# Kernel tuning notes

Measured on AMD Instinct MI355X. Metric: run time of the kernel, lower is better.

The kernel has to match this reference:

```python
import jax, jax.numpy as jnp
import numpy as np

D_MODEL = 512
N_PAIRS = D_MODEL // 2
B, T = 8, 4096


def setup_inputs() -> dict:
    key = jax.random.key(0)
    ks = jax.random.split(key, 7)
    scale = 1.0 / np.sqrt(D_MODEL)
    return {
        "x_seq": jax.random.normal(ks[0], (B, T, D_MODEL), dtype=jnp.float32),
        "W_angle": jax.random.uniform(ks[1], (D_MODEL, N_PAIRS), jnp.float32, -scale, scale),
        "b_angle": jnp.zeros((N_PAIRS,), jnp.float32),
        "W_decay": jax.random.uniform(ks[2], (D_MODEL, 1), jnp.float32, -scale, scale),
        "b_decay": jnp.full((1,), 1.4, jnp.float32),
        "W_input": jax.random.uniform(ks[3], (D_MODEL, D_MODEL), jnp.float32, -scale, scale),
        "b_input": jax.random.uniform(ks[4], (D_MODEL,), jnp.float32, -scale, scale),
    }


def _givens_ssm(x_seq, W_angle, b_angle, W_decay, b_decay, W_input, b_input):
    Bb, Tt, D = x_seq.shape
    P = D // 2
    angles = jnp.einsum("btd,dp->btp", x_seq, W_angle) + b_angle          # [B,T,P]
    decays = jax.nn.sigmoid(jnp.einsum("btd,dk->btk", x_seq, W_decay) + b_decay)[..., 0]  # [B,T]
    inj = jnp.einsum("btd,de->bte", x_seq, W_input) + b_input              # [B,T,D]
    inj = inj.reshape(Bb, Tt, P, 2)

    # scan over time: h_t = decay_t * Rot(angles_t) h_{t-1} + inj_t, pairwise 2x2 rotations
    def step(h, inp):
        a, d, u = inp  # a:[B,P], d:[B], u:[B,P,2]
        c, s = jnp.cos(a), jnp.sin(a)
        he = c * h[..., 0] - s * h[..., 1]
        ho = s * h[..., 0] + c * h[..., 1]
        h_new = d[:, None, None] * jnp.stack([he, ho], axis=-1) + u
        return h_new, h_new

    h0 = jnp.zeros((Bb, P, 2), x_seq.dtype)
    xs = (jnp.swapaxes(angles, 0, 1), jnp.swapaxes(decays, 0, 1), jnp.swapaxes(inj, 0, 1))
    _, states = jax.lax.scan(step, h0, xs)  # [T,B,P,2]
    return jnp.swapaxes(states, 0, 1).reshape(Bb, Tt, D)


def reference(x_seq, W_angle, b_angle, W_decay, b_decay, W_input, b_input):
    return _givens_ssm(x_seq, W_angle, b_angle, W_decay, b_decay, W_input, b_input)
```

## Files before the change

kernel.cpp:

```cpp
#include <hip/hip_runtime.h>
#include <math.h>

typedef _Float16 half_t;
typedef __attribute__((ext_vector_type(8))) _Float16 half8;
typedef __attribute__((ext_vector_type(4))) _Float16 half4;
typedef __attribute__((ext_vector_type(2))) _Float16 half2v;
typedef __attribute__((ext_vector_type(4))) float floatx4;

#define BATCH   8
#define SEQ     4096
#define DM      512
#define NP      256
#define M_TOT   32768
#define NTOT    768
#define CHUNKS  128
#define CHUNK_LEN 32

__device__ __forceinline__ void async_load16(const void* g, void* l) {
    __builtin_amdgcn_global_load_lds((const __attribute__((address_space(1))) void*)g,
                                     (__attribute__((address_space(3))) void*)l,
                                     16, 0, 0);
}

__global__ __launch_bounds__(256) void decay_convert(const float* __restrict__ X,
                                                     const float* __restrict__ Wd,
                                                     const float* __restrict__ bd,
                                                     float* __restrict__ dec,
                                                     half_t* __restrict__ Xh) {
    const int wave = threadIdx.x >> 6;
    const int lane = threadIdx.x & 63;
    const int row  = blockIdx.x * 4 + wave;
    const float4* xr = (const float4*)(X + (size_t)row * DM);
    const float4* wd = (const float4*)Wd;
    float4 v0 = xr[2 * lane], v1 = xr[2 * lane + 1];
    float4 w0 = wd[2 * lane], w1 = wd[2 * lane + 1];
    float sum = v0.x * w0.x + v0.y * w0.y + v0.z * w0.z + v0.w * w0.w
              + v1.x * w1.x + v1.y * w1.y + v1.z * w1.z + v1.w * w1.w;
    half8 h = {(half_t)v0.x, (half_t)v0.y, (half_t)v0.z, (half_t)v0.w,
               (half_t)v1.x, (half_t)v1.y, (half_t)v1.z, (half_t)v1.w};
    *(half8*)(Xh + (size_t)row * DM + lane * 8) = h;
#pragma unroll
    for (int off = 32; off > 0; off >>= 1) sum += __shfl_down(sum, off, 64);
    if (lane == 0) {
        float z = sum + bd[0];
        dec[row] = 1.0f / (1.0f + __expf(-z));
    }
}

__global__ __launch_bounds__(256) void wcat_transpose(const float* __restrict__ Wi,
                                                      const float* __restrict__ Wa,
                                                      half_t* __restrict__ Wt) {
    const int idx = blockIdx.x * 256 + threadIdx.x;
    const int n = idx >> 9;
    const int k = idx & 511;
    float v = (n < DM) ? Wi[(size_t)k * DM + n] : Wa[(size_t)k * NP + (n - DM)];
    Wt[idx] = (half_t)v;
}

__global__ __launch_bounds__(256) void gemm_fused(const half_t* __restrict__ Xh,
                                                  const half_t* __restrict__ Wt,
                                                  const float* __restrict__ bi,
                                                  const float* __restrict__ ba,
                                                  float* __restrict__ out,
                                                  half_t* __restrict__ angles) {
    __shared__ __align__(16) char As[2][8192];
    __shared__ __align__(16) char Bs[2][8192];

    const int bm   = blockIdx.x;
    const int bn   = blockIdx.y;
    const int tid  = threadIdx.x;
    const int wave = tid >> 6;
    const int lane = tid & 63;
    const int quad = lane >> 4;
    const int l16  = lane & 15;
    const int wrow = wave >> 1;
    const int wcol = wave & 1;

    floatx4 acc[4][4];
#pragma unroll
    for (int i = 0; i < 4; ++i)
#pragma unroll
        for (int j = 0; j < 4; ++j) acc[i][j] = (floatx4){0.f, 0.f, 0.f, 0.f};

    const int s0 = wave * 128 + lane;
    const int s1 = s0 + 64;
    const int r0 = s0 >> 2, kql0 = (s0 & 3) ^ ((r0 >> 1) & 3);
    const int r1 = s1 >> 2, kql1 = (s1 & 3) ^ ((r1 >> 1) & 3);
    const half_t* gA0 = Xh + (size_t)(bm * 128 + r0) * DM + kql0 * 8;
    const half_t* gA1 = Xh + (size_t)(bm * 128 + r1) * DM + kql1 * 8;
    const half_t* gB0 = Wt + (size_t)(bn * 128 + r0) * DM + kql0 * 8;
    const half_t* gB1 = Wt + (size_t)(bn * 128 + r1) * DM + kql1 * 8;

    for (int k0 = 0; k0 < DM; k0 += 64) {
#pragma unroll
        for (int kb = 0; kb < 2; ++kb) {
            const int ko = k0 + kb * 32;
            async_load16(gA0 + ko, As[kb] + wave * 2048);
            async_load16(gA1 + ko, As[kb] + wave * 2048 + 1024);
            async_load16(gB0 + ko, Bs[kb] + wave * 2048);
            async_load16(gB1 + ko, Bs[kb] + wave * 2048 + 1024);
        }
        __syncthreads();

#pragma unroll
        for (int kb = 0; kb < 2; ++kb) {
            half8 af[4], bf[4];
#pragma unroll
            for (int mt = 0; mt < 4; ++mt) {
                const int r = wrow * 64 + mt * 16 + l16;
                af[mt] = *(const half8*)(As[kb] + r * 64 + ((quad ^ ((r >> 1) & 3)) << 4));
            }
#pragma unroll
            for (int nt = 0; nt < 4; ++nt) {
                const int r = wcol * 64 + nt * 16 + l16;
                bf[nt] = *(const half8*)(Bs[kb] + r * 64 + ((quad ^ ((r >> 1) & 3)) << 4));
            }
#pragma unroll
            for (int mt = 0; mt < 4; ++mt)
#pragma unroll
                for (int nt = 0; nt < 4; ++nt)
                    acc[mt][nt] = __builtin_amdgcn_mfma_f32_16x16x32_f16(af[mt], bf[nt],
                                                                         acc[mt][nt], 0, 0, 0);
        }
        __syncthreads();
    }

    const int colbase = bn * 128 + wcol * 64;
#pragma unroll
    for (int nt = 0; nt < 4; ++nt) {
        const int col = colbase + nt * 16 + l16;
        const bool is_inj = col < DM;
        const float bias = is_inj ? bi[col] : ba[col - DM];
#pragma unroll
        for (int mt = 0; mt < 4; ++mt) {
            const int rowb = bm * 128 + wrow * 64 + mt * 16 + quad * 4;
#pragma unroll
            for (int r = 0; r < 4; ++r) {
                const float v = acc[mt][nt][r] + bias;
                const int row = rowb + r;
                if (is_inj) out[(size_t)row * DM + col] = v;
                else        angles[(size_t)row * NP + (col - DM)] = (half_t)v;
            }
        }
    }
}

__global__ __launch_bounds__(256) void scan_sum1(const half_t* __restrict__ angles,
                                                 const float* __restrict__ decays,
                                                 const float* __restrict__ inj,
                                                 float* __restrict__ thetaC,
                                                 float4* __restrict__ hend,
                                                 float* __restrict__ Dprod) {
    const int b    = blockIdx.x >> 6;
    const int sub  = threadIdx.x >> 7;
    const int th   = threadIdx.x & 127;
    const int c    = (blockIdx.x & 63) * 2 + sub;
    const int p0   = th * 2;
    const int t0   = c * CHUNK_LEN;
    const float4* inj4 = (const float4*)inj;

    float h0a = 0, h1a = 0, h0b = 0, h1b = 0, tha = 0, thb = 0, dc = 1.0f;
#pragma unroll 4
    for (int i = 0; i < CHUNK_LEN; ++i) {
        const int t = t0 + i;
        const size_t base = (size_t)(b * SEQ + t) * NP + p0;
        half2v av = *(const half2v*)(angles + base);
        float4 u = inj4[base >> 1];
        float d = decays[b * SEQ + t];
        float a0 = (float)av[0], a1 = (float)av[1];
        float s0, c0, s1, c1;
        __sincosf(a0, &s0, &c0);
        __sincosf(a1, &s1, &c1);
        float n0a = fmaf(d, c0 * h0a - s0 * h1a, u.x);
        float n1a = fmaf(d, s0 * h0a + c0 * h1a, u.y);
        float n0b = fmaf(d, c1 * h0b - s1 * h1b, u.z);
        float n1b = fmaf(d, s1 * h0b + c1 * h1b, u.w);
        h0a = n0a; h1a = n1a; h0b = n0b; h1b = n1b;
        tha += a0; thb += a1; dc *= d;
    }
    const size_t cbase = (size_t)(b * CHUNKS + c) * NP + p0;
    *(float2*)(thetaC + cbase) = make_float2(tha, thb);
    hend[cbase >> 1] = make_float4(h0a, h1a, h0b, h1b);
    if (th == 0) Dprod[b * CHUNKS + c] = dc;
}

__global__ __launch_bounds__(128) void scan_chunks(const float* __restrict__ thetaC,
                                                   const float4* __restrict__ hend,
                                                   const float* __restrict__ Dprod,
                                                   float4* __restrict__ hentry) {
    const int b  = blockIdx.x;
    const int p0 = threadIdx.x * 2;
    float h0a = 0, h1a = 0, h0b = 0, h1b = 0;
    for (int c = 0; c < CHUNKS; ++c) {
        const size_t cbase = (size_t)(b * CHUNKS + c) * NP + p0;
        hentry[cbase >> 1] = make_float4(h0a, h1a, h0b, h1b);
        float2 th2 = *(const float2*)(thetaC + cbase);
        float D = Dprod[b * CHUNKS + c];
        float4 he = hend[cbase >> 1];
        float s0, c0, s1, c1;
        __sincosf(th2.x, &s0, &c0);
        __sincosf(th2.y, &s1, &c1);
        float n0a = fmaf(D, c0 * h0a - s0 * h1a, he.x);
        float n1a = fmaf(D, s0 * h0a + c0 * h1a, he.y);
        float n0b = fmaf(D, c1 * h0b - s1 * h1b, he.z);
        float n1b = fmaf(D, s1 * h0b + c1 * h1b, he.w);
        h0a = n0a; h1a = n1a; h0b = n0b; h1b = n1b;
    }
}

__global__ __launch_bounds__(256) void scan_final(const half_t* __restrict__ angles,
                                                  const float* __restrict__ decays,
                                                  const float4* __restrict__ hentry,
                                                  float* __restrict__ out) {
    const int b    = blockIdx.x >> 6;
    const int sub  = threadIdx.x >> 7;
    const int th   = threadIdx.x & 127;
    const int c    = (blockIdx.x & 63) * 2 + sub;
    const int p0   = th * 2;
    const int t0   = c * CHUNK_LEN;
    float4* out4 = (float4*)out;

    float4 v = hentry[((size_t)(b * CHUNKS + c) * NP + p0) >> 1];
    float h0a = v.x, h1a = v.y, h0b = v.z, h1b = v.w;
#pragma unroll 4
    for (int i = 0; i < CHUNK_LEN; ++i) {
        const int t = t0 + i;
        const size_t base = (size_t)(b * SEQ + t) * NP + p0;
        half2v av = *(const half2v*)(angles + base);
        float4 u = out4[base >> 1];
        float d = decays[b * SEQ + t];
        float a0 = (float)av[0], a1 = (float)av[1];
        float s0, c0, s1, c1;
        __sincosf(a0, &s0, &c0);
        __sincosf(a1, &s1, &c1);
        float n0a = fmaf(d, c0 * h0a - s0 * h1a, u.x);
        float n1a = fmaf(d, s0 * h0a + c0 * h1a, u.y);
        float n0b = fmaf(d, c1 * h0b - s1 * h1b, u.z);
        float n1b = fmaf(d, s1 * h0b + c1 * h1b, u.w);
        h0a = n0a; h1a = n1a; h0b = n0b; h1b = n1b;
        out4[base >> 1] = make_float4(h0a, h1a, h0b, h1b);
    }
}

extern "C" void kernel_launch(void* const* d_in, const int* in_sizes, int n_in,
                              void* d_out, int out_size, void* d_ws, size_t ws_size,
                              hipStream_t stream) {
    const float* x  = (const float*)d_in[0];
    const float* Wa = (const float*)d_in[1];
    const float* ba = (const float*)d_in[2];
    const float* Wd = (const float*)d_in[3];
    const float* bd = (const float*)d_in[4];
    const float* Wi = (const float*)d_in[5];
    const float* bi = (const float*)d_in[6];
    float* out = (float*)d_out;

    char* ws = (char*)d_ws;
    half_t* x_h     = (half_t*)(ws);
    float*  thetaC  = (float*)(ws);
    float4* hend    = (float4*)(ws + 1048576);
    float*  Dprod   = (float*)(ws + 3145728);
    float4* hentry  = (float4*)(ws + 3149824);
    half_t* angles  = (half_t*)(ws + 33554432);
    float*  decays  = (float*)(ws + 50331648);
    half_t* Wcat_t  = (half_t*)(ws + 50462720);

    decay_convert<<<M_TOT / 4, 256, 0, stream>>>(x, Wd, bd, decays, x_h);
    wcat_transpose<<<(NTOT * DM) / 256, 256, 0, stream>>>(Wi, Wa, Wcat_t);
    gemm_fused<<<dim3(M_TOT / 128, NTOT / 128), 256, 0, stream>>>(x_h, Wcat_t, bi, ba, out, angles);

    scan_sum1<<<BATCH * CHUNKS / 2, 256, 0, stream>>>(angles, decays, out, thetaC, hend, Dprod);
    scan_chunks<<<BATCH, 128, 0, stream>>>(thetaC, hend, Dprod, hentry);
    scan_final<<<BATCH * CHUNKS / 2, 256, 0, stream>>>(angles, decays, hentry, out);
}
```

Before: 236.2 us.

## Prefetch scan inputs in register double-buffers, shrink GEMM LDS, two rows per wave

The three scan kernels now load their per-timestep inputs (angles, injections, decays, chunk summaries) in groups of 8 or 4 into register double-buffers, so global-load latency overlaps with the serial recurrence. The GEMM drops from a 64-wide K step with two LDS buffers to a 32-wide K step with one buffer per operand. That halves LDS use, but it also doubles the number of barriers. decay_convert now handles two rows per wave and launches half as many blocks. The prefetching raises register pressure in the scan kernels.

Result: faster. 221.4 us (-6.3%).

```diff
diff --git a/kernel.cpp b/kernel.cpp
--- a/kernel.cpp
+++ b/kernel.cpp
@@ -3,7 +3,6 @@
 
 typedef _Float16 half_t;
 typedef __attribute__((ext_vector_type(8))) _Float16 half8;
-typedef __attribute__((ext_vector_type(4))) _Float16 half4;
 typedef __attribute__((ext_vector_type(2))) _Float16 half2v;
 typedef __attribute__((ext_vector_type(4))) float floatx4;
 
@@ -29,21 +28,31 @@
                                                      half_t* __restrict__ Xh) {
     const int wave = threadIdx.x >> 6;
     const int lane = threadIdx.x & 63;
-    const int row  = blockIdx.x * 4 + wave;
-    const float4* xr = (const float4*)(X + (size_t)row * DM);
+    const int row0 = blockIdx.x * 8 + wave * 2;
+    const float4* x0 = (const float4*)(X + (size_t)row0 * DM);
+    const float4* x1 = x0 + 128;
     const float4* wd = (const float4*)Wd;
-    float4 v0 = xr[2 * lane], v1 = xr[2 * lane + 1];
+    float4 a0 = x0[2 * lane], a1 = x0[2 * lane + 1];
+    float4 b0 = x1[2 * lane], b1 = x1[2 * lane + 1];
     float4 w0 = wd[2 * lane], w1 = wd[2 * lane + 1];
-    float sum = v0.x * w0.x + v0.y * w0.y + v0.z * w0.z + v0.w * w0.w
-              + v1.x * w1.x + v1.y * w1.y + v1.z * w1.z + v1.w * w1.w;
-    half8 h = {(half_t)v0.x, (half_t)v0.y, (half_t)v0.z, (half_t)v0.w,
-               (half_t)v1.x, (half_t)v1.y, (half_t)v1.z, (half_t)v1.w};
-    *(half8*)(Xh + (size_t)row * DM + lane * 8) = h;
-#pragma unroll
-    for (int off = 32; off > 0; off >>= 1) sum += __shfl_down(sum, off, 64);
+    float s0 = a0.x * w0.x + a0.y * w0.y + a0.z * w0.z + a0.w * w0.w
+             + a1.x * w1.x + a1.y * w1.y + a1.z * w1.z + a1.w * w1.w;
+    float s1 = b0.x * w0.x + b0.y * w0.y + b0.z * w0.z + b0.w * w0.w
+             + b1.x * w1.x + b1.y * w1.y + b1.z * w1.z + b1.w * w1.w;
+    half8 h0 = {(half_t)a0.x, (half_t)a0.y, (half_t)a0.z, (half_t)a0.w,
+                (half_t)a1.x, (half_t)a1.y, (half_t)a1.z, (half_t)a1.w};
+    half8 h1 = {(half_t)b0.x, (half_t)b0.y, (half_t)b0.z, (half_t)b0.w,
+                (half_t)b1.x, (half_t)b1.y, (half_t)b1.z, (half_t)b1.w};
+    *(half8*)(Xh + (size_t)row0 * DM + lane * 8) = h0;
+    *(half8*)(Xh + (size_t)(row0 + 1) * DM + lane * 8) = h1;
+#pragma unroll
+    for (int off = 32; off > 0; off >>= 1) {
+        s0 += __shfl_down(s0, off, 64);
+        s1 += __shfl_down(s1, off, 64);
+    }
     if (lane == 0) {
-        float z = sum + bd[0];
-        dec[row] = 1.0f / (1.0f + __expf(-z));
+        dec[row0]     = 1.0f / (1.0f + __expf(-(s0 + bd[0])));
+        dec[row0 + 1] = 1.0f / (1.0f + __expf(-(s1 + bd[0])));
     }
 }
 
@@ -63,8 +72,8 @@
                                                   const float* __restrict__ ba,
                                                   float* __restrict__ out,
                                                   half_t* __restrict__ angles) {
-    __shared__ __align__(16) char As[2][8192];
-    __shared__ __align__(16) char Bs[2][8192];
+    __shared__ __align__(16) char As[8192];
+    __shared__ __align__(16) char Bs[8192];
 
     const int bm   = blockIdx.x;
     const int bn   = blockIdx.y;
@@ -90,38 +99,35 @@
     const half_t* gA1 = Xh + (size_t)(bm * 128 + r1) * DM + kql1 * 8;
     const half_t* gB0 = Wt + (size_t)(bn * 128 + r0) * DM + kql0 * 8;
     const half_t* gB1 = Wt + (size_t)(bn * 128 + r1) * DM + kql1 * 8;
-
-    for (int k0 = 0; k0 < DM; k0 += 64) {
-#pragma unroll
-        for (int kb = 0; kb < 2; ++kb) {
-            const int ko = k0 + kb * 32;
-            async_load16(gA0 + ko, As[kb] + wave * 2048);
-            async_load16(gA1 + ko, As[kb] + wave * 2048 + 1024);
-            async_load16(gB0 + ko, Bs[kb] + wave * 2048);
-            async_load16(gB1 + ko, Bs[kb] + wave * 2048 + 1024);
-        }
+    char* lA0 = As + wave * 2048;
+    char* lA1 = As + wave * 2048 + 1024;
+    char* lB0 = Bs + wave * 2048;
+    char* lB1 = Bs + wave * 2048 + 1024;
+
+    for (int k0 = 0; k0 < DM; k0 += 32) {
+        async_load16(gA0 + k0, lA0);
+        async_load16(gA1 + k0, lA1);
+        async_load16(gB0 + k0, lB0);
+        async_load16(gB1 + k0, lB1);
         __syncthreads();
 
-#pragma unroll
-        for (int kb = 0; kb < 2; ++kb) {
-            half8 af[4], bf[4];
-#pragma unroll
-            for (int mt = 0; mt < 4; ++mt) {
-                const int r = wrow * 64 + mt * 16 + l16;
-                af[mt] = *(const half8*)(As[kb] + r * 64 + ((quad ^ ((r >> 1) & 3)) << 4));
-            }
-#pragma unroll
-            for (int nt = 0; nt < 4; ++nt) {
-                const int r = wcol * 64 + nt * 16 + l16;
-                bf[nt] = *(const half8*)(Bs[kb] + r * 64 + ((quad ^ ((r >> 1) & 3)) << 4));
-            }
-#pragma unroll
-            for (int mt = 0; mt < 4; ++mt)
-#pragma unroll
-                for (int nt = 0; nt < 4; ++nt)
-                    acc[mt][nt] = __builtin_amdgcn_mfma_f32_16x16x32_f16(af[mt], bf[nt],
-                                                                         acc[mt][nt], 0, 0, 0);
-        }
+        half8 af[4], bf[4];
+#pragma unroll
+        for (int mt = 0; mt < 4; ++mt) {
+            const int r = wrow * 64 + mt * 16 + l16;
+            af[mt] = *(const half8*)(As + r * 64 + ((quad ^ ((r >> 1) & 3)) << 4));
+        }
+#pragma unroll
+        for (int nt = 0; nt < 4; ++nt) {
+            const int r = wcol * 64 + nt * 16 + l16;
+            bf[nt] = *(const half8*)(Bs + r * 64 + ((quad ^ ((r >> 1) & 3)) << 4));
+        }
+#pragma unroll
+        for (int mt = 0; mt < 4; ++mt)
+#pragma unroll
+            for (int nt = 0; nt < 4; ++nt)
+                acc[mt][nt] = __builtin_amdgcn_mfma_f32_16x16x32_f16(af[mt], bf[nt],
+                                                                     acc[mt][nt], 0, 0, 0);
         __syncthreads();
     }
 
@@ -151,32 +157,53 @@
                                                  float* __restrict__ thetaC,
                                                  float4* __restrict__ hend,
                                                  float* __restrict__ Dprod) {
-    const int b    = blockIdx.x >> 6;
-    const int sub  = threadIdx.x >> 7;
-    const int th   = threadIdx.x & 127;
-    const int c    = (blockIdx.x & 63) * 2 + sub;
-    const int p0   = th * 2;
-    const int t0   = c * CHUNK_LEN;
-    const float4* inj4 = (const float4*)inj;
+    const int b   = blockIdx.x >> 6;
+    const int sub = threadIdx.x >> 7;
+    const int th  = threadIdx.x & 127;
+    const int c   = (blockIdx.x & 63) * 2 + sub;
+    const int p0  = th * 2;
+    const int t0  = c * CHUNK_LEN;
+
+    const half_t* ap = angles + (size_t)(b * SEQ + t0) * NP + p0;
+    const float4* up = (const float4*)inj + (size_t)(b * SEQ + t0) * 128 + (p0 >> 1);
+    const float*  dp = decays + b * SEQ + t0;
+
+    half2v ab[2][8]; float4 ub[2][8]; float db[2][8];
+#pragma unroll
+    for (int j = 0; j < 8; ++j) {
+        ab[0][j] = *(const half2v*)(ap + (size_t)j * NP);
+        ub[0][j] = up[(size_t)j * 128];
+        db[0][j] = dp[j];
+    }
 
     float h0a = 0, h1a = 0, h0b = 0, h1b = 0, tha = 0, thb = 0, dc = 1.0f;
-#pragma unroll 4
-    for (int i = 0; i < CHUNK_LEN; ++i) {
-        const int t = t0 + i;
-        const size_t base = (size_t)(b * SEQ + t) * NP + p0;
-        half2v av = *(const half2v*)(angles + base);
-        float4 u = inj4[base >> 1];
-        float d = decays[b * SEQ + t];
-        float a0 = (float)av[0], a1 = (float)av[1];
-        float s0, c0, s1, c1;
-        __sincosf(a0, &s0, &c0);
-        __sincosf(a1, &s1, &c1);
-        float n0a = fmaf(d, c0 * h0a - s0 * h1a, u.x);
-        float n1a = fmaf(d, s0 * h0a + c0 * h1a, u.y);
-        float n0b = fmaf(d, c1 * h0b - s1 * h1b, u.z);
-        float n1b = fmaf(d, s1 * h0b + c1 * h1b, u.w);
-        h0a = n0a; h1a = n1a; h0b = n0b; h1b = n1b;
-        tha += a0; thb += a1; dc *= d;
+#pragma unroll
+    for (int g = 0; g < 4; ++g) {
+        const int cur = g & 1, nxt = cur ^ 1;
+        if (g < 3) {
+#pragma unroll
+            for (int j = 0; j < 8; ++j) {
+                const int t = (g + 1) * 8 + j;
+                ab[nxt][j] = *(const half2v*)(ap + (size_t)t * NP);
+                ub[nxt][j] = up[(size_t)t * 128];
+                db[nxt][j] = dp[t];
+            }
+        }
+#pragma unroll
+        for (int j = 0; j < 8; ++j) {
+            float a0 = (float)ab[cur][j][0], a1 = (float)ab[cur][j][1];
+            float4 u = ub[cur][j];
+            float d  = db[cur][j];
+            float s0, c0, s1, c1;
+            __sincosf(a0, &s0, &c0);
+            __sincosf(a1, &s1, &c1);
+            float n0a = fmaf(d, c0 * h0a - s0 * h1a, u.x);
+            float n1a = fmaf(d, s0 * h0a + c0 * h1a, u.y);
+            float n0b = fmaf(d, c1 * h0b - s1 * h1b, u.z);
+            float n1b = fmaf(d, s1 * h0b + c1 * h1b, u.w);
+            h0a = n0a; h1a = n1a; h0b = n0b; h1b = n1b;
+            tha += a0; thb += a1; dc *= d;
+        }
     }
     const size_t cbase = (size_t)(b * CHUNKS + c) * NP + p0;
     *(float2*)(thetaC + cbase) = make_float2(tha, thb);
@@ -190,21 +217,48 @@
                                                    float4* __restrict__ hentry) {
     const int b  = blockIdx.x;
     const int p0 = threadIdx.x * 2;
+    const float2* tp = (const float2*)thetaC + (size_t)b * CHUNKS * 128 + (p0 >> 1);
+    const float4* hp = hend + (size_t)b * CHUNKS * 128 + (p0 >> 1);
+    float4*       ep = hentry + (size_t)b * CHUNKS * 128 + (p0 >> 1);
+    const float*  Dp = Dprod + b * CHUNKS;
+
+    float2 tb[2][4]; float4 hb[2][4]; float Db[2][4];
+#pragma unroll
+    for (int j = 0; j < 4; ++j) {
+        tb[0][j] = tp[(size_t)j * 128];
+        hb[0][j] = hp[(size_t)j * 128];
+        Db[0][j] = Dp[j];
+    }
+
     float h0a = 0, h1a = 0, h0b = 0, h1b = 0;
-    for (int c = 0; c < CHUNKS; ++c) {
-        const size_t cbase = (size_t)(b * CHUNKS + c) * NP + p0;
-        hentry[cbase >> 1] = make_float4(h0a, h1a, h0b, h1b);
-        float2 th2 = *(const float2*)(thetaC + cbase);
-        float D = Dprod[b * CHUNKS + c];
-        float4 he = hend[cbase >> 1];
-        float s0, c0, s1, c1;
-        __sincosf(th2.x, &s0, &c0);
-        __sincosf(th2.y, &s1, &c1);
-        float n0a = fmaf(D, c0 * h0a - s0 * h1a, he.x);
-        float n1a = fmaf(D, s0 * h0a + c0 * h1a, he.y);
-        float n0b = fmaf(D, c1 * h0b - s1 * h1b, he.z);
-        float n1b = fmaf(D, s1 * h0b + c1 * h1b, he.w);
-        h0a = n0a; h1a = n1a; h0b = n0b; h1b = n1b;
+#pragma unroll
+    for (int g = 0; g < 32; ++g) {
+        const int cur = g & 1, nxt = cur ^ 1;
+        if (g < 31) {
+#pragma unroll
+            for (int j = 0; j < 4; ++j) {
+                const int c = (g + 1) * 4 + j;
+                tb[nxt][j] = tp[(size_t)c * 128];
+                hb[nxt][j] = hp[(size_t)c * 128];
+                Db[nxt][j] = Dp[c];
+            }
+        }
+#pragma unroll
+        for (int j = 0; j < 4; ++j) {
+            const int c = g * 4 + j;
+            ep[(size_t)c * 128] = make_float4(h0a, h1a, h0b, h1b);
+            float2 th2 = tb[cur][j];
+            float4 he  = hb[cur][j];
+            float D    = Db[cur][j];
+            float s0, c0, s1, c1;
+            __sincosf(th2.x, &s0, &c0);
+            __sincosf(th2.y, &s1, &c1);
+            float n0a = fmaf(D, c0 * h0a - s0 * h1a, he.x);
+            float n1a = fmaf(D, s0 * h0a + c0 * h1a, he.y);
+            float n0b = fmaf(D, c1 * h0b - s1 * h1b, he.z);
+            float n1b = fmaf(D, s1 * h0b + c1 * h1b, he.w);
+            h0a = n0a; h1a = n1a; h0b = n0b; h1b = n1b;
+        }
     }
 }
 
@@ -212,33 +266,56 @@
                                                   const float* __restrict__ decays,
                                                   const float4* __restrict__ hentry,
                                                   float* __restrict__ out) {
-    const int b    = blockIdx.x >> 6;
-    const int sub  = threadIdx.x >> 7;
-    const int th   = threadIdx.x & 127;
-    const int c    = (blockIdx.x & 63) * 2 + sub;
-    const int p0   = th * 2;
-    const int t0   = c * CHUNK_LEN;
-    float4* out4 = (float4*)out;
-
-    float4 v = hentry[((size_t)(b * CHUNKS + c) * NP + p0) >> 1];
+    const int b   = blockIdx.x >> 6;
+    const int sub = threadIdx.x >> 7;
+    const int th  = threadIdx.x & 127;
+    const int c   = (blockIdx.x & 63) * 2 + sub;
+    const int p0  = th * 2;
+    const int t0  = c * CHUNK_LEN;
+
+    const half_t* ap = angles + (size_t)(b * SEQ + t0) * NP + p0;
+    float4*       op = (float4*)out + (size_t)(b * SEQ + t0) * 128 + (p0 >> 1);
+    const float*  dp = decays + b * SEQ + t0;
+
+    float4 v = hentry[(size_t)(b * CHUNKS + c) * 128 + (p0 >> 1)];
     float h0a = v.x, h1a = v.y, h0b = v.z, h1b = v.w;
-#pragma unroll 4
-    for (int i = 0; i < CHUNK_LEN; ++i) {
-        const int t = t0 + i;
-        const size_t base = (size_t)(b * SEQ + t) * NP + p0;
-        half2v av = *(const half2v*)(angles + base);
-        float4 u = out4[base >> 1];
-        float d = decays[b * SEQ + t];
-        float a0 = (float)av[0], a1 = (float)av[1];
-        float s0, c0, s1, c1;
-        __sincosf(a0, &s0, &c0);
-        __sincosf(a1, &s1, &c1);
-        float n0a = fmaf(d, c0 * h0a - s0 * h1a, u.x);
-        float n1a = fmaf(d, s0 * h0a + c0 * h1a, u.y);
-        float n0b = fmaf(d, c1 * h0b - s1 * h1b, u.z);
-        float n1b = fmaf(d, s1 * h0b + c1 * h1b, u.w);
-        h0a = n0a; h1a = n1a; h0b = n0b; h1b = n1b;
-        out4[base >> 1] = make_float4(h0a, h1a, h0b, h1b);
+
+    half2v ab[2][8]; float4 ub[2][8]; float db[2][8];
+#pragma unroll
+    for (int j = 0; j < 8; ++j) {
+        ab[0][j] = *(const half2v*)(ap + (size_t)j * NP);
+        ub[0][j] = op[(size_t)j * 128];
+        db[0][j] = dp[j];
+    }
+
+#pragma unroll
+    for (int g = 0; g < 4; ++g) {
+        const int cur = g & 1, nxt = cur ^ 1;
+        if (g < 3) {
+#pragma unroll
+            for (int j = 0; j < 8; ++j) {
+                const int t = (g + 1) * 8 + j;
+                ab[nxt][j] = *(const half2v*)(ap + (size_t)t * NP);
+                ub[nxt][j] = op[(size_t)t * 128];
+                db[nxt][j] = dp[t];
+            }
+        }
+#pragma unroll
+        for (int j = 0; j < 8; ++j) {
+            const int t = g * 8 + j;
+            float a0 = (float)ab[cur][j][0], a1 = (float)ab[cur][j][1];
+            float4 u = ub[cur][j];
+            float d  = db[cur][j];
+            float s0, c0, s1, c1;
+            __sincosf(a0, &s0, &c0);
+            __sincosf(a1, &s1, &c1);
+            float n0a = fmaf(d, c0 * h0a - s0 * h1a, u.x);
+            float n1a = fmaf(d, s0 * h0a + c0 * h1a, u.y);
+            float n0b = fmaf(d, c1 * h0b - s1 * h1b, u.z);
+            float n1b = fmaf(d, s1 * h0b + c1 * h1b, u.w);
+            h0a = n0a; h1a = n1a; h0b = n0b; h1b = n1b;
+            op[(size_t)t * 128] = make_float4(h0a, h1a, h0b, h1b);
+        }
     }
 }
 
@@ -264,7 +341,7 @@
     float*  decays  = (float*)(ws + 50331648);
     half_t* Wcat_t  = (half_t*)(ws + 50462720);
 
-    decay_convert<<<M_TOT / 4, 256, 0, stream>>>(x, Wd, bd, decays, x_h);
+    decay_convert<<<M_TOT / 8, 256, 0, stream>>>(x, Wd, bd, decays, x_h);
     wcat_transpose<<<(NTOT * DM) / 256, 256, 0, stream>>>(Wi, Wa, Wcat_t);
     gemm_fused<<<dim3(M_TOT / 128, NTOT / 128), 256, 0, stream>>>(x_h, Wcat_t, bi, ba, out, angles);
 
```
